# Performance work log

Measured on AMD Instinct MI355X. Metric: run time of the kernel, lower is better.

Reference implementation:

```python
import jax, jax.numpy as jnp
import numpy as np

FP16_MAX = 65504.0  # clamp_fp16 bound
GROUP = 64          # SVDQuant int4 group size along in_features


def _int4_quant_dequant(w):
    """Symmetric per-(out_channel, group) int4 fake-quant of a weight [out, in].
    Emulates the W4 weight numerics of SVDQW4A4Linear at the dequantized level."""
    o, i = w.shape
    wg = w.reshape(o, i // GROUP, GROUP)
    scale = np.max(np.abs(wg), axis=-1, keepdims=True) / 7.0
    scale = np.where(scale == 0.0, 1.0, scale)
    q = np.clip(np.round(wg / scale), -8, 7)
    return (q * scale).reshape(o, i).astype(np.float32)


def setup_inputs() -> dict:
    dim, hidden = 3072, 8192
    B, S = 2, 4096
    rng = np.random.default_rng(0)
    # fused [w1; w3] weight: [2*hidden, dim]; down proj w2: [dim, hidden]
    w13 = _int4_quant_dequant((rng.standard_normal((2 * hidden, dim)) * 0.02).astype(np.float32))
    w2 = _int4_quant_dequant((rng.standard_normal((dim, hidden)) * 0.02).astype(np.float32))
    key = jax.random.key(0)
    x = jax.random.normal(key, (B, S, dim), dtype=jnp.float32)
    return {"x": x, "w13": jnp.asarray(w13), "w2": jnp.asarray(w2)}


def reference(x, w13, w2):
    # fused gate/up projection: [B,S,dim] @ [2H,dim]^T -> [B,S,2H]
    h = jnp.einsum("bsd,hd->bsh", x, w13)
    # NOTE: original code does `x3, x1 = x.chunk(2, dim=-1)` -> first half is x3
    x3, x1 = jnp.split(h, 2, axis=-1)
    g = jnp.clip(jax.nn.silu(x1) * x3, -FP16_MAX, FP16_MAX)  # clamp_fp16
    # down projection: [B,S,H] @ [dim,H]^T -> [B,S,dim]
    return jnp.einsum("bsh,dh->bsd", g, w2)
```

## Files before the change

kernel.cpp:

```cpp
#include <hip/hip_runtime.h>
#include <hip/hip_bf16.h>


typedef __attribute__((ext_vector_type(8))) __bf16 bf16x8;
typedef __attribute__((ext_vector_type(4))) float f32x4;

#define GLD_LDS16(gptr, lptr)                                                        \
  __builtin_amdgcn_global_load_lds(                                                  \
      (const __attribute__((address_space(1))) void*)(gptr),                         \
      (__attribute__((address_space(3))) void*)(lptr), 16, 0, 0)

#define VMCNT(n) asm volatile("s_waitcnt vmcnt(" #n ")" ::: "memory")
#define BAR()    __builtin_amdgcn_s_barrier()

#define MFMA16(a, b, c) __builtin_amdgcn_mfma_f32_16x16x32_bf16((a), (b), (c), 0, 0, 0)

__device__ __forceinline__ __bf16 bfr(float f) {
  unsigned int u = __builtin_bit_cast(unsigned int, f);
  unsigned short r = (unsigned short)((u + 0x7FFFu + ((u >> 16) & 1u)) >> 16);
  return __builtin_bit_cast(__bf16, r);
}

__global__ __launch_bounds__(256)
void k_cvt(const float* __restrict__ src, unsigned short* __restrict__ dst, long n) {
  long i = ((long)blockIdx.x * 256 + threadIdx.x) * 8;
  const long stride = (long)gridDim.x * 256 * 8;
  for (; i < n; i += stride) {
    float4 f0 = *(const float4*)(src + i);
    float4 f1 = *(const float4*)(src + i + 4);
    bf16x8 o;
    o[0] = bfr(f0.x); o[1] = bfr(f0.y); o[2] = bfr(f0.z); o[3] = bfr(f0.w);
    o[4] = bfr(f1.x); o[5] = bfr(f1.y); o[6] = bfr(f1.z); o[7] = bfr(f1.w);
    *(bf16x8*)(dst + i) = o;
  }
}

__global__ __launch_bounds__(512, 2)
void k_gateup14(const unsigned short* __restrict__ X,
                const unsigned short* __restrict__ W13,
                __hip_bfloat16* __restrict__ G)
{
  constexpr int K = 3072, LDG = 8192, NT = K / 64;
  __shared__ unsigned short lds[73728];

  const int t = threadIdx.x, l = t & 63, wid = t >> 6;
  const int wm = wid >> 2, wn = wid & 3;
  const int l15 = l & 15, lhi = l >> 4, sw = l15 & 7;

  const int bid = blockIdx.x;
  const int swz = (bid & 7) * 512 + (bid >> 3);
  const int mb = swz >> 6, nb = swz & 63;

  const int srow = t >> 3;
  const int scol = ((t & 7) ^ (srow & 7)) * 8;
  const unsigned short* xa = X   + (size_t)(mb * 128 + srow) * K + scol;
  const unsigned short* b3 = W13 + (size_t)(nb * 128 + srow) * K + scol;
  const unsigned short* b1 = W13 + (size_t)(8192 + nb * 128 + srow) * K + scol;
  const int lo = t * 8;

#define GST_A(e, kt) do {                                                       \
    GLD_LDS16(xa + (kt),                  lds + (e) * 24576 + lo);              \
    GLD_LDS16(xa + (size_t)64 * K + (kt),  lds + (e) * 24576 + 4096 + lo);      \
  } while (0)
#define GST_B3(e, kt) do {                                                      \
    GLD_LDS16(b3 + (kt),                  lds + (e) * 24576 + 8192 + lo);       \
    GLD_LDS16(b3 + (size_t)64 * K + (kt),  lds + (e) * 24576 + 12288 + lo);     \
  } while (0)
#define GST_B1(e, kt) do {                                                      \
    GLD_LDS16(b1 + (kt),                  lds + (e) * 24576 + 16384 + lo);      \
    GLD_LDS16(b1 + (size_t)64 * K + (kt),  lds + (e) * 24576 + 20480 + lo);     \
  } while (0)

  f32x4 acc3[4][2], acc1[4][2];
#pragma unroll
  for (int m = 0; m < 4; ++m)
#pragma unroll
    for (int n = 0; n < 2; ++n) {
      acc3[m][n] = (f32x4){0.f, 0.f, 0.f, 0.f};
      acc1[m][n] = (f32x4){0.f, 0.f, 0.f, 0.f};
    }

  GST_A(0, 0);  GST_B3(0, 0);  GST_B1(0, 0);
  GST_A(1, 64); GST_B3(1, 64); GST_B1(1, 64);

  for (int c = 0; c < NT; ++c) {
    const int e = c % 3;
    const int eS = (c + 2) % 3;
    const int k2 = (c + 2 < NT ? c + 2 : 0) * 64;
    const int Ab = e * 24576, B3b = Ab + 8192, B1b = Ab + 16384;

    VMCNT(6);
    BAR();

    bf16x8 ra[4][2], r3[2][2], r1[2][2];
#pragma unroll
    for (int mf = 0; mf < 4; ++mf)
#pragma unroll
      for (int kk = 0; kk < 2; ++kk) {
        const int row = wm * 64 + mf * 16 + l15;
        ra[mf][kk] = *(const bf16x8*)(lds + Ab + row * 64 + ((kk * 4 + lhi) ^ sw) * 8);
      }
#pragma unroll
    for (int nf = 0; nf < 2; ++nf)
#pragma unroll
      for (int kk = 0; kk < 2; ++kk) {
        const int row = wn * 32 + nf * 16 + l15;
        r3[nf][kk] = *(const bf16x8*)(lds + B3b + row * 64 + ((kk * 4 + lhi) ^ sw) * 8);
        r1[nf][kk] = *(const bf16x8*)(lds + B1b + row * 64 + ((kk * 4 + lhi) ^ sw) * 8);
      }

    GST_A(eS, k2); GST_B3(eS, k2); GST_B1(eS, k2);

    __builtin_amdgcn_s_setprio(1);
#pragma unroll
    for (int mf = 0; mf < 4; ++mf)
#pragma unroll
      for (int nf = 0; nf < 2; ++nf)
#pragma unroll
        for (int kk = 0; kk < 2; ++kk) {
          acc3[mf][nf] = MFMA16(ra[mf][kk], r3[nf][kk], acc3[mf][nf]);
          acc1[mf][nf] = MFMA16(ra[mf][kk], r1[nf][kk], acc1[mf][nf]);
        }
    __builtin_amdgcn_s_setprio(0);
  }

  const int gr0 = mb * 128 + wm * 64;
  const int gc0 = nb * 128 + wn * 32;
#pragma unroll
  for (int mf = 0; mf < 4; ++mf)
#pragma unroll
    for (int nf = 0; nf < 2; ++nf)
#pragma unroll
      for (int r = 0; r < 4; ++r) {
        float h3 = acc3[mf][nf][r];
        float h1 = acc1[mf][nf][r];
        float s  = h1 / (1.f + __expf(-h1));
        float g  = fminf(fmaxf(s * h3, -65504.f), 65504.f);
        G[(size_t)(gr0 + mf * 16 + lhi * 4 + r) * LDG + (gc0 + nf * 16 + l15)] =
            __float2bfloat16(g);
      }
#undef GST_A
#undef GST_B3
#undef GST_B1
}

__global__ __launch_bounds__(512, 2)
void k_down11(const unsigned short* __restrict__ Gm,
              const unsigned short* __restrict__ W2,
              float* __restrict__ Out)
{
  constexpr int K = 8192, LDO = 3072, NT = K / 64;
  __shared__ unsigned short lds[73728];

  const int t = threadIdx.x, l = t & 63, wid = t >> 6;
  const int wm = wid >> 1, wn = wid & 1;
  const int l15 = l & 15, lhi = l >> 4, sw = l15 & 7;

  const int bid = blockIdx.x;
  const int swz = (bid & 7) * 96 + (bid >> 3);
  const int mb = swz / 24, nb = swz % 24;

  const int srow = t >> 3;
  const int scol = ((t & 7) ^ (srow & 7)) * 8;
  const unsigned short* ga = Gm + (size_t)(mb * 256 + srow) * K + scol;
  const unsigned short* wb = W2 + (size_t)(nb * 128 + srow) * K + scol;
  const int lo = t * 8;

#define DST_A(e, kt) do {                                                       \
    GLD_LDS16(ga + (kt),                 lds + (e) * 16384 + lo);               \
    GLD_LDS16(ga + (size_t)64 * K + (kt),  lds + (e) * 16384 + 4096 + lo);      \
    GLD_LDS16(ga + (size_t)128 * K + (kt), lds + (e) * 16384 + 8192 + lo);      \
    GLD_LDS16(ga + (size_t)192 * K + (kt), lds + (e) * 16384 + 12288 + lo);     \
  } while (0)
#define DST_B(e, kt) do {                                                       \
    GLD_LDS16(wb + (kt),                lds + 49152 + (e) * 8192 + lo);         \
    GLD_LDS16(wb + (size_t)64 * K + (kt), lds + 49152 + (e) * 8192 + 4096 + lo); \
  } while (0)

  f32x4 acc[4][4];
#pragma unroll
  for (int mf = 0; mf < 4; ++mf)
#pragma unroll
    for (int nf = 0; nf < 4; ++nf)
      acc[mf][nf] = (f32x4){0.f, 0.f, 0.f, 0.f};

  DST_B(0, 0);  DST_A(0, 0);
  DST_B(1, 64); DST_A(1, 64);

  for (int c = 0; c < NT; ++c) {
    const int e = c % 3;
    const int eS = (c + 2) % 3;
    const int k2 = (c + 2 < NT ? c + 2 : 0) * 64;

    VMCNT(6);
    BAR();

    bf16x8 ra[4][2], rb[4][2];
#pragma unroll
    for (int mf = 0; mf < 4; ++mf)
#pragma unroll
      for (int kk = 0; kk < 2; ++kk)
        ra[mf][kk] = *(const bf16x8*)(lds + e * 16384 + (wm * 64 + mf * 16 + l15) * 64 + ((kk * 4 + lhi) ^ sw) * 8);
#pragma unroll
    for (int nf = 0; nf < 4; ++nf)
#pragma unroll
      for (int kk = 0; kk < 2; ++kk)
        rb[nf][kk] = *(const bf16x8*)(lds + 49152 + e * 8192 + (wn * 64 + nf * 16 + l15) * 64 + ((kk * 4 + lhi) ^ sw) * 8);

    DST_B(eS, k2);
    DST_A(eS, k2);

    __builtin_amdgcn_s_setprio(1);
#pragma unroll
    for (int mf = 0; mf < 4; ++mf)
#pragma unroll
      for (int nf = 0; nf < 4; ++nf)
#pragma unroll
        for (int kk = 0; kk < 2; ++kk)
          acc[mf][nf] = MFMA16(ra[mf][kk], rb[nf][kk], acc[mf][nf]);
    __builtin_amdgcn_s_setprio(0);
  }

  const int r0 = mb * 256 + wm * 64;
  const int c0 = nb * 128 + wn * 64;
#pragma unroll
  for (int mf = 0; mf < 4; ++mf)
#pragma unroll
    for (int nf = 0; nf < 4; ++nf)
#pragma unroll
      for (int r = 0; r < 4; ++r)
        Out[(size_t)(r0 + mf * 16 + lhi * 4 + r) * LDO + (c0 + nf * 16 + l15)] =
            acc[mf][nf][r];
#undef DST_A
#undef DST_B
}

extern "C" void kernel_launch(void* const* d_in, const int* in_sizes, int n_in,
                              void* d_out, int out_size, void* d_ws, size_t ws_size,
                              hipStream_t stream) {
  const float* x   = (const float*)d_in[0];
  const float* w13 = (const float*)d_in[1];
  const float* w2  = (const float*)d_in[2];
  float* out = (float*)d_out;

  const long NX = 25165824L, NW13 = 50331648L, NW2 = 25165824L;
  const size_t XB = 50331648, W13B = 100663296, W2B = 50331648;

  unsigned short* xb   = (unsigned short*)d_ws;
  unsigned short* w13b = (unsigned short*)((char*)d_ws + XB);
  unsigned short* w2b  = (unsigned short*)((char*)d_ws + XB + W13B);
  __hip_bfloat16* g    = (__hip_bfloat16*)((char*)d_ws + XB + W13B + W2B);

  k_cvt<<<2048, 256, 0, stream>>>(x,   xb,   NX);
  k_cvt<<<2048, 256, 0, stream>>>(w13, w13b, NW13);
  k_cvt<<<2048, 256, 0, stream>>>(w2,  w2b,  NW2);
  k_gateup14<<<4096, 512, 0, stream>>>(xb, w13b, g);
  k_down11<<<768, 512, 0, stream>>>((const unsigned short*)g, w2b, out);
}
```

Baseline: 1.397 ms.

## Load gate-up A operand directly to registers and double the M tile

The gate/up GEMM now reads the activation (A) fragments straight from global memory into registers instead of staging them through LDS. Each block now covers 256 rows instead of 128, with 8 M-fragments per warp, and the grid is halved. Only the W1/W3 tiles still go through the triple-buffered LDS pipeline, which shrinks shared memory use. The risks are higher register pressure from doubling the accumulators and A registers, uncoalesced direct global reads of A, and exposed load latency, since the next k-step's A loads are issued inside the MFMA loop.

Result: slower. 2.200 ms (+57.4%).

```diff
diff --git a/kernel.cpp b/kernel.cpp
--- a/kernel.cpp
+++ b/kernel.cpp
@@ -36,98 +36,96 @@
 }
 
 __global__ __launch_bounds__(512, 2)
-void k_gateup14(const unsigned short* __restrict__ X,
+void k_gateup15(const unsigned short* __restrict__ X,
                 const unsigned short* __restrict__ W13,
                 __hip_bfloat16* __restrict__ G)
 {
   constexpr int K = 3072, LDG = 8192, NT = K / 64;
-  __shared__ unsigned short lds[73728];
+  __shared__ unsigned short lds[49152];
 
   const int t = threadIdx.x, l = t & 63, wid = t >> 6;
   const int wm = wid >> 2, wn = wid & 3;
   const int l15 = l & 15, lhi = l >> 4, sw = l15 & 7;
 
   const int bid = blockIdx.x;
-  const int swz = (bid & 7) * 512 + (bid >> 3);
+  const int swz = (bid & 7) * 256 + (bid >> 3);
   const int mb = swz >> 6, nb = swz & 63;
+
+  const unsigned short* ap = X + (size_t)(mb * 256 + wm * 128 + l15) * K + lhi * 8;
 
   const int srow = t >> 3;
   const int scol = ((t & 7) ^ (srow & 7)) * 8;
-  const unsigned short* xa = X   + (size_t)(mb * 128 + srow) * K + scol;
   const unsigned short* b3 = W13 + (size_t)(nb * 128 + srow) * K + scol;
   const unsigned short* b1 = W13 + (size_t)(8192 + nb * 128 + srow) * K + scol;
   const int lo = t * 8;
 
-#define GST_A(e, kt) do {                                                       \
-    GLD_LDS16(xa + (kt),                  lds + (e) * 24576 + lo);              \
-    GLD_LDS16(xa + (size_t)64 * K + (kt),  lds + (e) * 24576 + 4096 + lo);      \
+#define STB(e, kt) do {                                                        \
+    GLD_LDS16(b3 + (kt),                 lds + (e) * 16384 + lo);              \
+    GLD_LDS16(b3 + (size_t)64 * K + (kt), lds + (e) * 16384 + 4096 + lo);      \
+    GLD_LDS16(b1 + (kt),                 lds + (e) * 16384 + 8192 + lo);       \
+    GLD_LDS16(b1 + (size_t)64 * K + (kt), lds + (e) * 16384 + 12288 + lo);     \
   } while (0)
-#define GST_B3(e, kt) do {                                                      \
-    GLD_LDS16(b3 + (kt),                  lds + (e) * 24576 + 8192 + lo);       \
-    GLD_LDS16(b3 + (size_t)64 * K + (kt),  lds + (e) * 24576 + 12288 + lo);     \
-  } while (0)
-#define GST_B1(e, kt) do {                                                      \
-    GLD_LDS16(b1 + (kt),                  lds + (e) * 24576 + 16384 + lo);      \
-    GLD_LDS16(b1 + (size_t)64 * K + (kt),  lds + (e) * 24576 + 20480 + lo);     \
-  } while (0)
-
-  f32x4 acc3[4][2], acc1[4][2];
-#pragma unroll
-  for (int m = 0; m < 4; ++m)
+
+  f32x4 acc3[8][2], acc1[8][2];
+#pragma unroll
+  for (int m = 0; m < 8; ++m)
 #pragma unroll
     for (int n = 0; n < 2; ++n) {
       acc3[m][n] = (f32x4){0.f, 0.f, 0.f, 0.f};
       acc1[m][n] = (f32x4){0.f, 0.f, 0.f, 0.f};
     }
 
-  GST_A(0, 0);  GST_B3(0, 0);  GST_B1(0, 0);
-  GST_A(1, 64); GST_B3(1, 64); GST_B1(1, 64);
+  bf16x8 aa[8][2];
+#pragma unroll
+  for (int mf = 0; mf < 8; ++mf)
+#pragma unroll
+    for (int kk = 0; kk < 2; ++kk)
+      aa[mf][kk] = *(const bf16x8*)(ap + (size_t)(mf * 16) * K + kk * 32);
+  STB(0, 0);
+  STB(1, 64);
 
   for (int c = 0; c < NT; ++c) {
     const int e = c % 3;
     const int eS = (c + 2) % 3;
-    const int k2 = (c + 2 < NT ? c + 2 : 0) * 64;
-    const int Ab = e * 24576, B3b = Ab + 8192, B1b = Ab + 16384;
-
-    VMCNT(6);
+    const int k2 = (c + 2 < NT ? c + 2 : c + 2 - NT) * 64;
+    const int kn = (c + 1 < NT ? c + 1 : 0) * 64;
+    const int Bb = e * 16384;
+
+    VMCNT(4);
     BAR();
 
-    bf16x8 ra[4][2], r3[2][2], r1[2][2];
-#pragma unroll
-    for (int mf = 0; mf < 4; ++mf)
-#pragma unroll
-      for (int kk = 0; kk < 2; ++kk) {
-        const int row = wm * 64 + mf * 16 + l15;
-        ra[mf][kk] = *(const bf16x8*)(lds + Ab + row * 64 + ((kk * 4 + lhi) ^ sw) * 8);
-      }
+    bf16x8 r3[2][2], r1[2][2];
 #pragma unroll
     for (int nf = 0; nf < 2; ++nf)
 #pragma unroll
       for (int kk = 0; kk < 2; ++kk) {
         const int row = wn * 32 + nf * 16 + l15;
-        r3[nf][kk] = *(const bf16x8*)(lds + B3b + row * 64 + ((kk * 4 + lhi) ^ sw) * 8);
-        r1[nf][kk] = *(const bf16x8*)(lds + B1b + row * 64 + ((kk * 4 + lhi) ^ sw) * 8);
+        r3[nf][kk] = *(const bf16x8*)(lds + Bb + row * 64 + ((kk * 4 + lhi) ^ sw) * 8);
+        r1[nf][kk] = *(const bf16x8*)(lds + Bb + 8192 + row * 64 + ((kk * 4 + lhi) ^ sw) * 8);
       }
 
-    GST_A(eS, k2); GST_B3(eS, k2); GST_B1(eS, k2);
-
     __builtin_amdgcn_s_setprio(1);
 #pragma unroll
-    for (int mf = 0; mf < 4; ++mf)
+    for (int mf = 0; mf < 8; ++mf) {
 #pragma unroll
       for (int nf = 0; nf < 2; ++nf)
 #pragma unroll
         for (int kk = 0; kk < 2; ++kk) {
-          acc3[mf][nf] = MFMA16(ra[mf][kk], r3[nf][kk], acc3[mf][nf]);
-          acc1[mf][nf] = MFMA16(ra[mf][kk], r1[nf][kk], acc1[mf][nf]);
+          acc3[mf][nf] = MFMA16(aa[mf][kk], r3[nf][kk], acc3[mf][nf]);
+          acc1[mf][nf] = MFMA16(aa[mf][kk], r1[nf][kk], acc1[mf][nf]);
         }
+      aa[mf][0] = *(const bf16x8*)(ap + (size_t)(mf * 16) * K + kn);
+      aa[mf][1] = *(const bf16x8*)(ap + (size_t)(mf * 16) * K + 32 + kn);
+    }
     __builtin_amdgcn_s_setprio(0);
+
+    STB(eS, k2);
   }
 
-  const int gr0 = mb * 128 + wm * 64;
+  const int gr0 = mb * 256 + wm * 128;
   const int gc0 = nb * 128 + wn * 32;
 #pragma unroll
-  for (int mf = 0; mf < 4; ++mf)
+  for (int mf = 0; mf < 8; ++mf)
 #pragma unroll
     for (int nf = 0; nf < 2; ++nf)
 #pragma unroll
@@ -139,9 +137,7 @@
         G[(size_t)(gr0 + mf * 16 + lhi * 4 + r) * LDG + (gc0 + nf * 16 + l15)] =
             __float2bfloat16(g);
       }
-#undef GST_A
-#undef GST_B3
-#undef GST_B1
+#undef STB
 }
 
 __global__ __launch_bounds__(512, 2)
@@ -254,6 +250,6 @@
   k_cvt<<<2048, 256, 0, stream>>>(x,   xb,   NX);
   k_cvt<<<2048, 256, 0, stream>>>(w13, w13b, NW13);
   k_cvt<<<2048, 256, 0, stream>>>(w2,  w2b,  NW2);
-  k_gateup14<<<4096, 512, 0, stream>>>(xb, w13b, g);
+  k_gateup15<<<2048, 512, 0, stream>>>(xb, w13b, g);
   k_down11<<<768, 512, 0, stream>>>((const unsigned short*)g, w2b, out);
 }
```
